# Optimization experiments

Hardware: AMD Instinct MI355X
Metric: run time of the kernel (lower is better)

## Reference

```python
import jax, jax.numpy as jnp
import numpy as np

EMBED_DIM = 768
NUM_HEADS = 12
HEAD_DIM = EMBED_DIM // NUM_HEADS


def setup_inputs() -> dict:
    key = jax.random.key(0)
    k1, k2, k3, k4, k5 = jax.random.split(key, 5)
    x = jax.random.normal(k1, (2, 4096, EMBED_DIM), dtype=jnp.float32)
    # nn.Linear(embedding_dim, 3*embedding_dim): weight [3d, d], bias [3d]
    w_qkv = jax.random.normal(k2, (3 * EMBED_DIM, EMBED_DIM), dtype=jnp.float32) * (1.0 / np.sqrt(EMBED_DIM))
    b_qkv = jax.random.normal(k3, (3 * EMBED_DIM,), dtype=jnp.float32) * 0.02
    # LayerNorm affine params
    ln_gamma = jnp.ones((EMBED_DIM,), dtype=jnp.float32)
    ln_beta = jnp.zeros((EMBED_DIM,), dtype=jnp.float32)
    return {"x": x, "w_qkv": w_qkv, "b_qkv": b_qkv, "ln_gamma": ln_gamma, "ln_beta": ln_beta}


def _layernorm(x, gamma, beta, eps=1e-5):
    mu = jnp.mean(x, axis=-1, keepdims=True)
    var = jnp.var(x, axis=-1, keepdims=True)
    return (x - mu) * jax.lax.rsqrt(var + eps) * gamma + beta


def reference(x, w_qkv, b_qkv, ln_gamma, ln_beta):
    b, n, d = x.shape
    h, hd = NUM_HEADS, HEAD_DIM
    qkv = x @ w_qkv.T + b_qkv                      # [b, n, 3d]
    qkv = qkv.reshape(b, n, 3, h, hd)
    qkv = jnp.transpose(qkv, (2, 0, 3, 1, 4))      # [3, b, h, n, hd]
    Q, K, V = qkv[0], qkv[1], qkv[2]
    scale = 1.0 / np.sqrt(hd).astype(np.float32)
    scores = jnp.einsum('bhqd,bhkd->bhqk', Q, K) * scale   # [b, h, n, n]
    attn = jax.nn.softmax(scores, axis=-1)
    out = jnp.einsum('bhqk,bhkd->bhqd', attn, V)           # [b, h, n, hd]
    out = jnp.transpose(out, (0, 2, 1, 3)).reshape(b, n, d)
    return _layernorm(x + out, ln_gamma, ln_beta)
```

## Files before the change

### kernel.cpp

```cpp
#include <hip/hip_runtime.h>
#include <stdint.h>

#define NUM_HEADS 12
#define HEAD_DIM 64
#define EMB 768
#define SEQ 4096
#define BATCH 2
#define ROWS (BATCH*SEQ)
#define DQKV (3*EMB)

typedef __attribute__((ext_vector_type(8))) __bf16 bf16x8;
typedef __attribute__((ext_vector_type(4))) float floatx4;

static __device__ __forceinline__ unsigned short f2bf(float f) {
  unsigned int u = __float_as_uint(f);
  u += 0x7FFFu + ((u >> 16) & 1u);
  return (unsigned short)(u >> 16);
}

static __device__ __forceinline__ float bf2f(unsigned short h) {
  return __uint_as_float(((unsigned int)h) << 16);
}

static __device__ __forceinline__ unsigned int pack_bf2_trunc(float a, float b) {
  return __builtin_amdgcn_perm(__float_as_uint(b), __float_as_uint(a), 0x07060302u);
}

static __device__ __forceinline__ void async_cp16(void* lds, const void* g) {
  __builtin_amdgcn_global_load_lds(
      (__attribute__((address_space(1))) void*)(g),
      (__attribute__((address_space(3))) void*)(lds), 16, 0, 0);
}

static __device__ __forceinline__ int perm_key(int nn) {
  return (nn & ~31) | (((nn >> 2) & 3) * 8 + ((nn >> 4) & 1) * 4 + (nn & 3));
}

#define N4X (ROWS*EMB/4)
#define N4W (DQKV*EMB/4)
__global__ __launch_bounds__(256) void cvt2_kernel(
    const float* __restrict__ x, const float* __restrict__ w,
    unsigned short* __restrict__ xb, unsigned short* __restrict__ wb) {
  int i = blockIdx.x * blockDim.x + threadIdx.x;
  const float4* src;
  ushort4* dst;
  if (i < N4X) { src = (const float4*)x; dst = (ushort4*)xb; }
  else { i -= N4X; if (i >= N4W) return; src = (const float4*)w; dst = (ushort4*)wb; }
  float4 v = src[i];
  ushort4 o;
  o.x = f2bf(v.x); o.y = f2bf(v.y); o.z = f2bf(v.z); o.w = f2bf(v.w);
  dst[i] = o;
}

__global__ __launch_bounds__(256) void qkv_gemm_kernel(
    const unsigned short* __restrict__ xb, const unsigned short* __restrict__ wb,
    const float* __restrict__ bias,
    unsigned short* __restrict__ Qb, unsigned short* __restrict__ Kb,
    unsigned short* __restrict__ Vt) {
  __shared__ unsigned short As[128 * 64];
  __shared__ unsigned short Bs[128 * 64];
  const int t = threadIdx.x;
  const int lane = t & 63;
  const int w = t >> 6;
  const int wm = w >> 1, wn = w & 1;
  const int fr = lane & 15, fq = lane >> 4;
  const int fx = fr & 7;
  const int m0 = blockIdx.x * 128;
  const int n0 = blockIdx.y * 128;
  const int sel = n0 / EMB;
  const int lr = t >> 3;
  const int sc = t & 7;

  floatx4 acc[4][4];
#pragma unroll
  for (int i = 0; i < 4; ++i)
#pragma unroll
    for (int j = 0; j < 4; ++j) acc[i][j] = (floatx4)(0.0f);

  if (sel < 2) {
    for (int k0 = 0; k0 < EMB; k0 += 64) {
      __syncthreads();
#pragma unroll
      for (int i = 0; i < 4; ++i) {
        const int rr = i*32 + lr;
        const int cg = ((sc ^ (lr & 7)) * 8);
        async_cp16(&As[rr*64 + sc*8], &xb[(size_t)(m0 + rr)*EMB + k0 + cg]);
        async_cp16(&Bs[rr*64 + sc*8], &wb[(size_t)(n0 + rr)*EMB + k0 + cg]);
      }
      __syncthreads();
#pragma unroll
      for (int ks = 0; ks < 2; ++ks) {
        bf16x8 af[4], bfr[4];
#pragma unroll
        for (int i = 0; i < 4; ++i)
          af[i] = *(const bf16x8*)&As[(wm*64 + i*16 + fr)*64 + (((ks*4+fq) ^ fx)*8)];
#pragma unroll
        for (int j = 0; j < 4; ++j)
          bfr[j] = *(const bf16x8*)&Bs[(wn*64 + j*16 + fr)*64 + (((ks*4+fq) ^ fx)*8)];
#pragma unroll
        for (int i = 0; i < 4; ++i)
#pragma unroll
          for (int j = 0; j < 4; ++j)
            acc[i][j] = __builtin_amdgcn_mfma_f32_16x16x32_bf16(bfr[j], af[i], acc[i][j], 0, 0, 0);
      }
    }
    const float qscale = 0.125f * 1.4426950408889634f;
    const float sc2 = (sel == 0) ? qscale : 1.0f;
    unsigned short* dst = (sel == 0) ? Qb : Kb;
#pragma unroll
    for (int i = 0; i < 4; ++i) {
      const int mr = m0 + wm*64 + i*16 + fr;
      const int b = mr / SEQ;
      const int nn = mr - b*SEQ;
#pragma unroll
      for (int j = 0; j < 4; ++j) {
        const int og = n0 + wn*64 + j*16 + fq*4;
        const int oo = og - sel*EMB;
        const int hh = oo >> 6, dd = oo & 63;
        const float4 bv = *(const float4*)&bias[og];
        ushort4 pk;
        pk.x = f2bf((acc[i][j][0] + bv.x) * sc2);
        pk.y = f2bf((acc[i][j][1] + bv.y) * sc2);
        pk.z = f2bf((acc[i][j][2] + bv.z) * sc2);
        pk.w = f2bf((acc[i][j][3] + bv.w) * sc2);
        *(ushort4*)&dst[(((size_t)(b*NUM_HEADS + hh))*SEQ + nn)*HEAD_DIM + dd] = pk;
      }
    }
  } else {
    for (int k0 = 0; k0 < EMB; k0 += 64) {
      __syncthreads();
#pragma unroll
      for (int i = 0; i < 4; ++i) {
        const int rr = i*32 + lr;
        const int cg = ((sc ^ (lr & 7)) * 8);
        async_cp16(&As[rr*64 + sc*8], &xb[(size_t)(m0 + rr)*EMB + k0 + cg]);
        async_cp16(&Bs[rr*64 + sc*8], &wb[(size_t)(n0 + rr)*EMB + k0 + cg]);
      }
      __syncthreads();
#pragma unroll
      for (int ks = 0; ks < 2; ++ks) {
        bf16x8 af[4], bfr[4];
#pragma unroll
        for (int i = 0; i < 4; ++i)
          af[i] = *(const bf16x8*)&As[(wm*64 + i*16 + fr)*64 + (((ks*4+fq) ^ fx)*8)];
#pragma unroll
        for (int j = 0; j < 4; ++j)
          bfr[j] = *(const bf16x8*)&Bs[(wn*64 + j*16 + fr)*64 + (((ks*4+fq) ^ fx)*8)];
#pragma unroll
        for (int i = 0; i < 4; ++i)
#pragma unroll
          for (int j = 0; j < 4; ++j)
            acc[i][j] = __builtin_amdgcn_mfma_f32_16x16x32_bf16(af[i], bfr[j], acc[i][j], 0, 0, 0);
      }
    }
#pragma unroll
    for (int i = 0; i < 4; ++i) {
      const int mr = m0 + wm*64 + i*16 + fq*4;
      const int b = mr / SEQ;
      const int nn = perm_key(mr - b*SEQ);
#pragma unroll
      for (int j = 0; j < 4; ++j) {
        const int feat = n0 + wn*64 + j*16 + fr;
        const int oo = feat - 2*EMB;
        const int hh = oo >> 6, dd = oo & 63;
        const float bv = bias[feat];
        ushort4 pk;
        pk.x = f2bf(acc[i][j][0] + bv);
        pk.y = f2bf(acc[i][j][1] + bv);
        pk.z = f2bf(acc[i][j][2] + bv);
        pk.w = f2bf(acc[i][j][3] + bv);
        *(ushort4*)&Vt[(((size_t)(b*NUM_HEADS + hh))*HEAD_DIM + dd)*SEQ + nn] = pk;
      }
    }
  }
}

#define NT (SEQ/64)
__global__ __launch_bounds__(256, 4) void attn_kernel(
    const unsigned short* __restrict__ Qb, const unsigned short* __restrict__ Kb,
    const unsigned short* __restrict__ Vt, unsigned short* __restrict__ Oo) {
  __shared__ unsigned short Ks[2][64 * 64];
  __shared__ unsigned short Vs[2][64 * 64];
  const int t = threadIdx.x;
  const int lane = t & 63;
  const int w = t >> 6;
  const int fr = lane & 15, fq = lane >> 4;
  const int fx = fr & 7;
  const int bh = blockIdx.y;
  const int q0 = blockIdx.x * 128 + w * 32;

  bf16x8 aq[2][2];
#pragma unroll
  for (int g = 0; g < 2; ++g) {
    const size_t qoff = ((size_t)bh * SEQ + q0 + g*16 + fr) * HEAD_DIM;
    aq[g][0] = *(const bf16x8*)&Qb[qoff + fq*8];
    aq[g][1] = *(const bf16x8*)&Qb[qoff + 32 + fq*8];
  }

  union { unsigned int u[4]; bf16x8 b; } onesu;
  onesu.u[0] = onesu.u[1] = onesu.u[2] = onesu.u[3] = 0x3F803F80u;
  const bf16x8 onesb = onesu.b;

  floatx4 o[2][4];
  floatx4 lsum[2];
#pragma unroll
  for (int g = 0; g < 2; ++g) {
    lsum[g] = (floatx4)(0.f);
#pragma unroll
    for (int d = 0; d < 4; ++d) o[g][d] = (floatx4)(0.f);
  }

  const size_t kb = (size_t)bh * SEQ * HEAD_DIM;
  const size_t vb = (size_t)bh * HEAD_DIM * SEQ;

  auto stage = [&](int kc, int bi) {
#pragma unroll
    for (int i = 0; i < 2; ++i) {
      const int chunk = i*256 + t;
      const int r = chunk >> 3, c = chunk & 7;
      async_cp16(&Ks[bi][chunk*8], &Kb[kb + (size_t)(kc + r)*HEAD_DIM + ((c ^ (r&7))*8)]);
    }
#pragma unroll
    for (int i = 0; i < 2; ++i) {
      const int chunk = i*256 + t;
      const int r = chunk >> 3, c = chunk & 7;
      async_cp16(&Vs[bi][chunk*8], &Vt[vb + (size_t)r*SEQ + kc + ((c ^ (r&7))*8)]);
    }
  };

  auto sfrag = [&](const unsigned short* ksp, int J2, floatx4 (&zz)[2][2]) {
#pragma unroll
    for (int jj = 0; jj < 2; ++jj) {
      const int row = (J2*2 + jj)*16 + fr;
      bf16x8 k0 = *(const bf16x8*)&ksp[row*64 + ((fq ^ fx)*8)];
      bf16x8 k1 = *(const bf16x8*)&ksp[row*64 + (((fq+4) ^ fx)*8)];
#pragma unroll
      for (int g = 0; g < 2; ++g) {
        floatx4 a = (floatx4)(0.f);
        a = __builtin_amdgcn_mfma_f32_16x16x32_bf16(k0, aq[g][0], a, 0, 0, 0);
        a = __builtin_amdgcn_mfma_f32_16x16x32_bf16(k1, aq[g][1], a, 0, 0, 0);
        zz[g][jj] = a;
      }
    }
  };

  auto softmax_pv = [&](const unsigned short* vsp, int J, floatx4 (&zc)[2][2]) {
    bf16x8 ap[2];
#pragma unroll
    for (int g = 0; g < 2; ++g) {
      float e0 = __builtin_amdgcn_exp2f(zc[g][0][0]);
      float e1 = __builtin_amdgcn_exp2f(zc[g][0][1]);
      float e2 = __builtin_amdgcn_exp2f(zc[g][0][2]);
      float e3 = __builtin_amdgcn_exp2f(zc[g][0][3]);
      float e4 = __builtin_amdgcn_exp2f(zc[g][1][0]);
      float e5 = __builtin_amdgcn_exp2f(zc[g][1][1]);
      float e6 = __builtin_amdgcn_exp2f(zc[g][1][2]);
      float e7 = __builtin_amdgcn_exp2f(zc[g][1][3]);
      union { unsigned int u[4]; bf16x8 b; } cv;
      cv.u[0] = pack_bf2_trunc(e0, e1);
      cv.u[1] = pack_bf2_trunc(e2, e3);
      cv.u[2] = pack_bf2_trunc(e4, e5);
      cv.u[3] = pack_bf2_trunc(e6, e7);
      ap[g] = cv.b;
    }
    __builtin_amdgcn_s_setprio(1);
#pragma unroll
    for (int g = 0; g < 2; ++g)
      lsum[g] = __builtin_amdgcn_mfma_f32_16x16x32_bf16(ap[g], onesb, lsum[g], 0, 0, 0);
    const int vc = ((4*J + fq) ^ fx) * 8;
#pragma unroll
    for (int dt = 0; dt < 4; ++dt) {
      const bf16x8 vvb = *(const bf16x8*)&vsp[(dt*16 + fr)*64 + vc];
#pragma unroll
      for (int g = 0; g < 2; ++g)
        o[g][dt] = __builtin_amdgcn_mfma_f32_16x16x32_bf16(ap[g], vvb, o[g][dt], 0, 0, 0);
    }
    __builtin_amdgcn_s_setprio(0);
  };

  stage(0, 0);
  stage(64, 1);
  asm volatile("s_waitcnt vmcnt(4)" ::: "memory");
  __builtin_amdgcn_s_barrier();

  int cur = 0;
  for (int tt = 0; tt < NT; ++tt) {
    const unsigned short* ksp = Ks[cur];
    const unsigned short* vsp = Vs[cur];
    floatx4 z[2][2], zn[2][2];
    sfrag(ksp, 0, z);
    sfrag(ksp, 1, zn);
    softmax_pv(vsp, 0, z);
    softmax_pv(vsp, 1, zn);
    if (tt == NT - 1) break;
    __builtin_amdgcn_s_barrier();
    if (tt + 2 < NT) {
      stage((tt + 2) * 64, cur);
      asm volatile("s_waitcnt vmcnt(4)" ::: "memory");
    } else {
      asm volatile("s_waitcnt vmcnt(0)" ::: "memory");
    }
    __builtin_amdgcn_s_barrier();
    cur ^= 1;
  }

  const int b = bh / NUM_HEADS, hh = bh - b*NUM_HEADS;
#pragma unroll
  for (int g = 0; g < 2; ++g)
#pragma unroll
    for (int r4 = 0; r4 < 4; ++r4) {
      const float li = 1.0f / lsum[g][r4];
      const size_t obase = ((size_t)b*SEQ + q0 + g*16 + fq*4 + r4)*EMB + hh*HEAD_DIM;
#pragma unroll
      for (int dt = 0; dt < 4; ++dt)
        Oo[obase + dt*16 + fr] = f2bf(o[g][dt][r4] * li);
    }
}

__global__ __launch_bounds__(256) void ln_kernel(
    const float* __restrict__ x, const unsigned short* __restrict__ att,
    const float* __restrict__ gamma, const float* __restrict__ beta,
    float* __restrict__ out) {
  const int row = blockIdx.x * 4 + (threadIdx.x >> 6);
  const int lane = threadIdx.x & 63;
  const size_t base = (size_t)row * EMB;
  float4 v[3];
  float s = 0.f, s2 = 0.f;
#pragma unroll
  for (int k = 0; k < 3; ++k) {
    const int c = lane*4 + k*256;
    const float4 xv = *(const float4*)&x[base + c];
    const ushort4 a4 = *(const ushort4*)&att[base + c];
    v[k].x = xv.x + bf2f(a4.x);
    v[k].y = xv.y + bf2f(a4.y);
    v[k].z = xv.z + bf2f(a4.z);
    v[k].w = xv.w + bf2f(a4.w);
    s  += (v[k].x + v[k].y) + (v[k].z + v[k].w);
    s2 += (v[k].x*v[k].x + v[k].y*v[k].y) + (v[k].z*v[k].z + v[k].w*v[k].w);
  }
#pragma unroll
  for (int off = 1; off < 64; off <<= 1) {
    s  += __shfl_xor(s,  off);
    s2 += __shfl_xor(s2, off);
  }
  const float mean = s * (1.0f / EMB);
  const float var  = s2 * (1.0f / EMB) - mean * mean;
  const float rstd = rsqrtf(var + 1e-5f);
#pragma unroll
  for (int k = 0; k < 3; ++k) {
    const int c = lane*4 + k*256;
    const float4 g4 = *(const float4*)&gamma[c];
    const float4 b4 = *(const float4*)&beta[c];
    float4 ov;
    ov.x = (v[k].x - mean) * rstd * g4.x + b4.x;
    ov.y = (v[k].y - mean) * rstd * g4.y + b4.y;
    ov.z = (v[k].z - mean) * rstd * g4.z + b4.z;
    ov.w = (v[k].w - mean) * rstd * g4.w + b4.w;
    *(float4*)&out[base + c] = ov;
  }
}

extern "C" void kernel_launch(void* const* d_in, const int* in_sizes, int n_in,
                              void* d_out, int out_size, void* d_ws, size_t ws_size,
                              hipStream_t stream) {
  const float* x      = (const float*)d_in[0];
  const float* w_qkv  = (const float*)d_in[1];
  const float* b_qkv  = (const float*)d_in[2];
  const float* gamma  = (const float*)d_in[3];
  const float* beta   = (const float*)d_in[4];
  float* out = (float*)d_out;

  unsigned short* xb = (unsigned short*)d_ws;
  unsigned short* wb = xb + (size_t)ROWS * EMB;
  unsigned short* Qb = wb + (size_t)DQKV * EMB;
  unsigned short* Kb = Qb + (size_t)ROWS * EMB;
  unsigned short* Vt = Kb + (size_t)ROWS * EMB;
  unsigned short* att = Vt + (size_t)ROWS * EMB;

  cvt2_kernel<<<(N4X + N4W + 255)/256, 256, 0, stream>>>(x, w_qkv, xb, wb);
  qkv_gemm_kernel<<<dim3(ROWS/128, DQKV/128), 256, 0, stream>>>(xb, wb, b_qkv, Qb, Kb, Vt);
  attn_kernel<<<dim3(SEQ/128, BATCH*NUM_HEADS), 256, 0, stream>>>(Qb, Kb, Vt, att);
  ln_kernel<<<ROWS/4, 256, 0, stream>>>(x, att, gamma, beta, out);
}
```

Before: 252.7 us.

## Give each attention wave 64 query rows with 2-wave blocks to reuse K/V fragments

The attention block shrinks from 4 waves to 2, and each wave now handles 64 query rows (4 groups of 16) instead of 32. Every K/V fragment read from LDS is therefore reused across twice as many MFMAs, halving LDS reads per FLOP. The S and PV computations are merged into one per-chunk routine that preloads all V fragments and interleaves exp with the PV MFMAs. In exchange, register pressure roughly doubles (launch bounds drop to 2 blocks), fewer waves share each block's K/V staging, and occupancy and latency hiding may suffer.

Result: slower. 268.4 us (+6.2%).

```diff
diff --git a/kernel.cpp b/kernel.cpp
--- a/kernel.cpp
+++ b/kernel.cpp
@@ -176,7 +176,7 @@
 }
 
 #define NT (SEQ/64)
-__global__ __launch_bounds__(256, 4) void attn_kernel(
+__global__ __launch_bounds__(128, 2) void attn_kernel(
     const unsigned short* __restrict__ Qb, const unsigned short* __restrict__ Kb,
     const unsigned short* __restrict__ Vt, unsigned short* __restrict__ Oo) {
   __shared__ unsigned short Ks[2][64 * 64];
@@ -187,11 +187,11 @@
   const int fr = lane & 15, fq = lane >> 4;
   const int fx = fr & 7;
   const int bh = blockIdx.y;
-  const int q0 = blockIdx.x * 128 + w * 32;
-
-  bf16x8 aq[2][2];
-#pragma unroll
-  for (int g = 0; g < 2; ++g) {
+  const int q0 = blockIdx.x * 128 + w * 64;
+
+  bf16x8 aq[4][2];
+#pragma unroll
+  for (int g = 0; g < 4; ++g) {
     const size_t qoff = ((size_t)bh * SEQ + q0 + g*16 + fr) * HEAD_DIM;
     aq[g][0] = *(const bf16x8*)&Qb[qoff + fq*8];
     aq[g][1] = *(const bf16x8*)&Qb[qoff + 32 + fq*8];
@@ -201,10 +201,10 @@
   onesu.u[0] = onesu.u[1] = onesu.u[2] = onesu.u[3] = 0x3F803F80u;
   const bf16x8 onesb = onesu.b;
 
-  floatx4 o[2][4];
-  floatx4 lsum[2];
-#pragma unroll
-  for (int g = 0; g < 2; ++g) {
+  floatx4 o[4][4];
+  floatx4 lsum[4];
+#pragma unroll
+  for (int g = 0; g < 4; ++g) {
     lsum[g] = (floatx4)(0.f);
 #pragma unroll
     for (int d = 0; d < 4; ++d) o[g][d] = (floatx4)(0.f);
@@ -215,88 +215,81 @@
 
   auto stage = [&](int kc, int bi) {
 #pragma unroll
-    for (int i = 0; i < 2; ++i) {
-      const int chunk = i*256 + t;
+    for (int i = 0; i < 4; ++i) {
+      const int chunk = i*128 + t;
       const int r = chunk >> 3, c = chunk & 7;
       async_cp16(&Ks[bi][chunk*8], &Kb[kb + (size_t)(kc + r)*HEAD_DIM + ((c ^ (r&7))*8)]);
     }
 #pragma unroll
-    for (int i = 0; i < 2; ++i) {
-      const int chunk = i*256 + t;
+    for (int i = 0; i < 4; ++i) {
+      const int chunk = i*128 + t;
       const int r = chunk >> 3, c = chunk & 7;
       async_cp16(&Vs[bi][chunk*8], &Vt[vb + (size_t)r*SEQ + kc + ((c ^ (r&7))*8)]);
     }
   };
 
-  auto sfrag = [&](const unsigned short* ksp, int J2, floatx4 (&zz)[2][2]) {
+  auto chunk_compute = [&](const unsigned short* ksp, const unsigned short* vsp,
+                           int J) {
+    floatx4 z[4][2];
 #pragma unroll
     for (int jj = 0; jj < 2; ++jj) {
-      const int row = (J2*2 + jj)*16 + fr;
+      const int row = (J*2 + jj)*16 + fr;
       bf16x8 k0 = *(const bf16x8*)&ksp[row*64 + ((fq ^ fx)*8)];
       bf16x8 k1 = *(const bf16x8*)&ksp[row*64 + (((fq+4) ^ fx)*8)];
 #pragma unroll
-      for (int g = 0; g < 2; ++g) {
+      for (int g = 0; g < 4; ++g) {
         floatx4 a = (floatx4)(0.f);
         a = __builtin_amdgcn_mfma_f32_16x16x32_bf16(k0, aq[g][0], a, 0, 0, 0);
         a = __builtin_amdgcn_mfma_f32_16x16x32_bf16(k1, aq[g][1], a, 0, 0, 0);
-        zz[g][jj] = a;
-      }
-    }
-  };
-
-  auto softmax_pv = [&](const unsigned short* vsp, int J, floatx4 (&zc)[2][2]) {
-    bf16x8 ap[2];
-#pragma unroll
-    for (int g = 0; g < 2; ++g) {
-      float e0 = __builtin_amdgcn_exp2f(zc[g][0][0]);
-      float e1 = __builtin_amdgcn_exp2f(zc[g][0][1]);
-      float e2 = __builtin_amdgcn_exp2f(zc[g][0][2]);
-      float e3 = __builtin_amdgcn_exp2f(zc[g][0][3]);
-      float e4 = __builtin_amdgcn_exp2f(zc[g][1][0]);
-      float e5 = __builtin_amdgcn_exp2f(zc[g][1][1]);
-      float e6 = __builtin_amdgcn_exp2f(zc[g][1][2]);
-      float e7 = __builtin_amdgcn_exp2f(zc[g][1][3]);
+        z[g][jj] = a;
+      }
+    }
+    bf16x8 vvb[4];
+    const int vc = ((4*J + fq) ^ fx) * 8;
+#pragma unroll
+    for (int dt = 0; dt < 4; ++dt)
+      vvb[dt] = *(const bf16x8*)&vsp[(dt*16 + fr)*64 + vc];
+#pragma unroll
+    for (int g = 0; g < 4; ++g) {
+      float e0 = __builtin_amdgcn_exp2f(z[g][0][0]);
+      float e1 = __builtin_amdgcn_exp2f(z[g][0][1]);
+      float e2 = __builtin_amdgcn_exp2f(z[g][0][2]);
+      float e3 = __builtin_amdgcn_exp2f(z[g][0][3]);
+      float e4 = __builtin_amdgcn_exp2f(z[g][1][0]);
+      float e5 = __builtin_amdgcn_exp2f(z[g][1][1]);
+      float e6 = __builtin_amdgcn_exp2f(z[g][1][2]);
+      float e7 = __builtin_amdgcn_exp2f(z[g][1][3]);
       union { unsigned int u[4]; bf16x8 b; } cv;
       cv.u[0] = pack_bf2_trunc(e0, e1);
       cv.u[1] = pack_bf2_trunc(e2, e3);
       cv.u[2] = pack_bf2_trunc(e4, e5);
       cv.u[3] = pack_bf2_trunc(e6, e7);
-      ap[g] = cv.b;
-    }
-    __builtin_amdgcn_s_setprio(1);
-#pragma unroll
-    for (int g = 0; g < 2; ++g)
-      lsum[g] = __builtin_amdgcn_mfma_f32_16x16x32_bf16(ap[g], onesb, lsum[g], 0, 0, 0);
-    const int vc = ((4*J + fq) ^ fx) * 8;
-#pragma unroll
-    for (int dt = 0; dt < 4; ++dt) {
-      const bf16x8 vvb = *(const bf16x8*)&vsp[(dt*16 + fr)*64 + vc];
-#pragma unroll
-      for (int g = 0; g < 2; ++g)
-        o[g][dt] = __builtin_amdgcn_mfma_f32_16x16x32_bf16(ap[g], vvb, o[g][dt], 0, 0, 0);
-    }
-    __builtin_amdgcn_s_setprio(0);
+      const bf16x8 ap = cv.b;
+      __builtin_amdgcn_s_setprio(1);
+      lsum[g] = __builtin_amdgcn_mfma_f32_16x16x32_bf16(ap, onesb, lsum[g], 0, 0, 0);
+#pragma unroll
+      for (int dt = 0; dt < 4; ++dt)
+        o[g][dt] = __builtin_amdgcn_mfma_f32_16x16x32_bf16(ap, vvb[dt], o[g][dt], 0, 0, 0);
+      __builtin_amdgcn_s_setprio(0);
+    }
   };
 
   stage(0, 0);
   stage(64, 1);
-  asm volatile("s_waitcnt vmcnt(4)" ::: "memory");
+  asm volatile("s_waitcnt vmcnt(8)" ::: "memory");
   __builtin_amdgcn_s_barrier();
 
   int cur = 0;
   for (int tt = 0; tt < NT; ++tt) {
     const unsigned short* ksp = Ks[cur];
     const unsigned short* vsp = Vs[cur];
-    floatx4 z[2][2], zn[2][2];
-    sfrag(ksp, 0, z);
-    sfrag(ksp, 1, zn);
-    softmax_pv(vsp, 0, z);
-    softmax_pv(vsp, 1, zn);
+    chunk_compute(ksp, vsp, 0);
+    chunk_compute(ksp, vsp, 1);
     if (tt == NT - 1) break;
     __builtin_amdgcn_s_barrier();
     if (tt + 2 < NT) {
       stage((tt + 2) * 64, cur);
-      asm volatile("s_waitcnt vmcnt(4)" ::: "memory");
+      asm volatile("s_waitcnt vmcnt(8)" ::: "memory");
     } else {
       asm volatile("s_waitcnt vmcnt(0)" ::: "memory");
     }
@@ -306,7 +299,7 @@
 
   const int b = bh / NUM_HEADS, hh = bh - b*NUM_HEADS;
 #pragma unroll
-  for (int g = 0; g < 2; ++g)
+  for (int g = 0; g < 4; ++g)
 #pragma unroll
     for (int r4 = 0; r4 < 4; ++r4) {
       const float li = 1.0f / lsum[g][r4];
@@ -379,6 +372,6 @@
 
   cvt2_kernel<<<(N4X + N4W + 255)/256, 256, 0, stream>>>(x, w_qkv, xb, wb);
   qkv_gemm_kernel<<<dim3(ROWS/128, DQKV/128), 256, 0, stream>>>(xb, wb, b_qkv, Qb, Kb, Vt);
-  attn_kernel<<<dim3(SEQ/128, BATCH*NUM_HEADS), 256, 0, stream>>>(Qb, Kb, Vt, att);
+  attn_kernel<<<dim3(SEQ/128, BATCH*NUM_HEADS), 128, 0, stream>>>(Qb, Kb, Vt, att);
   ln_kernel<<<ROWS/4, 256, 0, stream>>>(x, att, gamma, beta, out);
 }
```
